# Kernel tuning notes

Hardware: AMD Instinct MI355X
Metric: run time of the kernel (lower is better)

## Reference

```python
import jax, jax.numpy as jnp
import numpy as np

N, D = 8192, 256
NUM_CLASSES = 100
WEIGHT = 1.0


def setup_inputs() -> dict:
    key = jax.random.key(0)
    k1, k2 = jax.random.split(key)
    predictions = jax.random.normal(k1, (N, D), dtype=jnp.float32)
    targets = jax.random.randint(k2, (N,), 0, NUM_CLASSES, dtype=jnp.int32)
    return {"predictions": predictions, "targets": targets}


def reference(predictions, targets):
    # Pairwise squared L2 via ||a||^2 + ||b||^2 - 2 a.b  -> [N, N]
    sq = jnp.sum(predictions * predictions, axis=1)
    d2 = sq[:, None] + sq[None, :] - 2.0 * (predictions @ predictions.T)
    dist = jnp.sqrt(jnp.maximum(d2, 0.0))  # torch.dist(p=2)

    n = predictions.shape[0]
    upper = jnp.triu(jnp.ones((n, n), dtype=bool), k=1)  # i < j pairs only
    same = targets[:, None] == targets[None, :]
    mask = upper & same

    num = jnp.sum(mask).astype(dist.dtype)
    loss = jnp.sum(jnp.where(mask, dist, 0.0)) / num
    return loss * WEIGHT
```

## Files before the change

### kernel.cpp

```cpp
#include <hip/hip_runtime.h>

#define N_CLS 100
#define D_DIM 256
#define MAX_M 112
#define ROW_SH 264
#define PANEL 48

typedef short bf16x8 __attribute__((ext_vector_type(8)));
typedef float f32x4  __attribute__((ext_vector_type(4)));

__device__ __forceinline__ unsigned short f2bf(float f) {
    unsigned int b = __float_as_uint(f);
    return (unsigned short)((b + 0x7FFFu + ((b >> 16) & 1u)) >> 16);
}

__global__ __launch_bounds__(1024) void k_prep(const int* __restrict__ targets, int n,
        int* __restrict__ offsets, int* __restrict__ bucket,
        double* __restrict__ npairs, double* __restrict__ gsum, int* __restrict__ gcount) {
    __shared__ int h[N_CLS], cur[N_CLS], offs[N_CLS + 1];
    const int t = threadIdx.x;
    if (t < N_CLS) h[t] = 0;
    __syncthreads();
    for (int i = t; i < n; i += 1024) atomicAdd(&h[targets[i]], 1);
    __syncthreads();
    if (t == 0) {
        int acc = 0; double p = 0.0;
        offs[0] = 0;
        for (int c = 0; c < N_CLS; ++c) {
            int m = h[c]; acc += m; offs[c + 1] = acc;
            p += (double)m * (double)(m - 1) * 0.5;
        }
        *npairs = p; *gsum = 0.0; *gcount = 0;
    }
    __syncthreads();
    if (t <= N_CLS) offsets[t] = offs[t];
    if (t < N_CLS) cur[t] = offs[t];
    __syncthreads();
    for (int i = t; i < n; i += 1024) {
        int c = targets[i];
        int pos = atomicAdd(&cur[c], 1);
        bucket[pos] = i;
    }
}

__device__ __forceinline__ void stage(const float* __restrict__ pred,
        const int* __restrict__ bucket, int base, int m, int cp0, int dslot, int cnt,
        short* tileS, float* sqs, int wave, int lane) {
    for (int r = wave; r < cnt; r += 8) {
        int cp = cp0 + r;
        float4 v = make_float4(0.f, 0.f, 0.f, 0.f);
        if (cp < m) {
            int g = bucket[base + cp];
            v = ((const float4*)(pred + (size_t)g * D_DIM))[lane];
        }
        short4 pk;
        pk.x = (short)f2bf(v.x); pk.y = (short)f2bf(v.y);
        pk.z = (short)f2bf(v.z); pk.w = (short)f2bf(v.w);
        *(short4*)&tileS[(dslot + r) * ROW_SH + lane * 4] = pk;
        float s = v.x * v.x + v.y * v.y + v.z * v.z + v.w * v.w;
        #pragma unroll
        for (int o = 32; o; o >>= 1) s += __shfl_xor(s, o, 64);
        if (lane == 0) sqs[dslot + r] = s;
    }
}

__device__ __forceinline__ float tile16(const short* tileS, const float* sqs,
        int a0, int b0, int ga0, int gb0, int m, int lane) {
    const int q = lane >> 4, l15 = lane & 15;
    const short* aP = &tileS[(a0 + l15) * ROW_SH + q * 8];
    const short* bP = &tileS[(b0 + l15) * ROW_SH + q * 8];
    f32x4 acc = {0.f, 0.f, 0.f, 0.f};
    #pragma unroll
    for (int ks = 0; ks < 8; ++ks) {
        bf16x8 af = *(const bf16x8*)(aP + ks * 32);
        bf16x8 bg = *(const bf16x8*)(bP + ks * 32);
        acc = __builtin_amdgcn_mfma_f32_16x16x32_bf16(af, bg, acc, 0, 0, 0);
    }
    float out = 0.f;
    #pragma unroll
    for (int rr = 0; rr < 4; ++rr) {
        int al = q * 4 + rr;
        int pi = ga0 + al, pj = gb0 + l15;
        float d2 = sqs[a0 + al] + sqs[b0 + l15] - 2.f * acc[rr];
        if (pj < m && pi < pj) out += sqrtf(fmaxf(d2, 0.f));
    }
    return out;
}

__global__ __launch_bounds__(512) void k_gram(const float* __restrict__ pred,
        const int* __restrict__ bucket, const int* __restrict__ offsets,
        const double* __restrict__ npairs, double* __restrict__ gsum,
        int* __restrict__ gcount, float* __restrict__ out) {
    __shared__ short tileS[MAX_M * ROW_SH];
    __shared__ float sqs[MAX_M];
    __shared__ float wsum[8];
    const int t = threadIdx.x, lane = t & 63, wave = t >> 6;
    const int c = blockIdx.x;
    const int base = offsets[c];
    const int m = offsets[c + 1] - base;
    float accum = 0.f;

    if (m <= MAX_M) {
        const int T = (m + 15) >> 4;
        stage(pred, bucket, base, m, 0, 0, T * 16, tileS, sqs, wave, lane);
        __syncthreads();
        const int np = T * (T + 1) / 2;
        for (int idx = wave; idx < np; idx += 8) {
            int ta = 0, r = idx;
            while (r >= T - ta) { r -= T - ta; ++ta; }
            int tb = ta + r;
            accum += tile16(tileS, sqs, ta * 16, tb * 16, ta * 16, tb * 16, m, lane);
        }
    } else {
        const int P = (m + PANEL - 1) / PANEL;
        for (int pi = 0; pi < P; ++pi)
        for (int pj = pi; pj < P; ++pj) {
            __syncthreads();
            stage(pred, bucket, base, m, pi * PANEL, 0,     PANEL, tileS, sqs, wave, lane);
            stage(pred, bucket, base, m, pj * PANEL, PANEL, PANEL, tileS, sqs, wave, lane);
            __syncthreads();
            for (int idx = wave; idx < 9; idx += 8) {
                int ta = idx / 3, tb = idx % 3;
                accum += tile16(tileS, sqs, ta * 16, PANEL + tb * 16,
                                pi * PANEL + ta * 16, pj * PANEL + tb * 16, m, lane);
            }
        }
    }

    #pragma unroll
    for (int o = 32; o; o >>= 1) accum += __shfl_xor(accum, o, 64);
    if (lane == 0) wsum[wave] = accum;
    __syncthreads();
    if (t == 0) {
        double bs = 0.0;
        #pragma unroll
        for (int w = 0; w < 8; ++w) bs += (double)wsum[w];
        atomicAdd(gsum, bs);
        __threadfence();
        int ticket = atomicAdd(gcount, 1);
        if (ticket == (int)gridDim.x - 1) {
            __threadfence();
            double s = atomicAdd(gsum, 0.0);
            out[0] = (float)(s / *npairs);
        }
    }
}

extern "C" void kernel_launch(void* const* d_in, const int* in_sizes, int n_in,
                              void* d_out, int out_size, void* d_ws, size_t ws_size,
                              hipStream_t stream) {
    const float* pred  = (const float*)d_in[0];
    const int* targets = (const int*)d_in[1];
    float* out         = (float*)d_out;
    const int n = in_sizes[1];

    char* ws = (char*)d_ws;
    size_t off = 0;
    double* npairs  = (double*)(ws + off); off += 8;
    double* gsum    = (double*)(ws + off); off += 8;
    int*    gcount  = (int*)(ws + off);    off += 8;
    int*    offsets = (int*)(ws + off);    off += (N_CLS + 1) * 4;
    int*    bucket  = (int*)(ws + off);

    k_prep<<<1, 1024, 0, stream>>>(targets, n, offsets, bucket, npairs, gsum, gcount);
    k_gram<<<N_CLS, 512, 0, stream>>>(pred, bucket, offsets, npairs, gsum, gcount, out);
}
```

Baseline: 80.09 us.

## Fold class bucketing into per-class gram blocks and add a final reduction kernel

```diff
diff --git a/kernel.cpp b/kernel.cpp
--- a/kernel.cpp
+++ b/kernel.cpp
@@ -14,43 +14,14 @@
     return (unsigned short)((b + 0x7FFFu + ((b >> 16) & 1u)) >> 16);
 }
 
-__global__ __launch_bounds__(1024) void k_prep(const int* __restrict__ targets, int n,
-        int* __restrict__ offsets, int* __restrict__ bucket,
-        double* __restrict__ npairs, double* __restrict__ gsum, int* __restrict__ gcount) {
-    __shared__ int h[N_CLS], cur[N_CLS], offs[N_CLS + 1];
-    const int t = threadIdx.x;
-    if (t < N_CLS) h[t] = 0;
-    __syncthreads();
-    for (int i = t; i < n; i += 1024) atomicAdd(&h[targets[i]], 1);
-    __syncthreads();
-    if (t == 0) {
-        int acc = 0; double p = 0.0;
-        offs[0] = 0;
-        for (int c = 0; c < N_CLS; ++c) {
-            int m = h[c]; acc += m; offs[c + 1] = acc;
-            p += (double)m * (double)(m - 1) * 0.5;
-        }
-        *npairs = p; *gsum = 0.0; *gcount = 0;
-    }
-    __syncthreads();
-    if (t <= N_CLS) offsets[t] = offs[t];
-    if (t < N_CLS) cur[t] = offs[t];
-    __syncthreads();
-    for (int i = t; i < n; i += 1024) {
-        int c = targets[i];
-        int pos = atomicAdd(&cur[c], 1);
-        bucket[pos] = i;
-    }
-}
-
 __device__ __forceinline__ void stage(const float* __restrict__ pred,
-        const int* __restrict__ bucket, int base, int m, int cp0, int dslot, int cnt,
+        const int* __restrict__ bkt, int m, int cp0, int dslot, int cnt,
         short* tileS, float* sqs, int wave, int lane) {
     for (int r = wave; r < cnt; r += 8) {
         int cp = cp0 + r;
         float4 v = make_float4(0.f, 0.f, 0.f, 0.f);
         if (cp < m) {
-            int g = bucket[base + cp];
+            int g = bkt[cp];
             v = ((const float4*)(pred + (size_t)g * D_DIM))[lane];
         }
         short4 pk;
@@ -88,21 +59,27 @@
 }
 
 __global__ __launch_bounds__(512) void k_gram(const float* __restrict__ pred,
-        const int* __restrict__ bucket, const int* __restrict__ offsets,
-        const double* __restrict__ npairs, double* __restrict__ gsum,
-        int* __restrict__ gcount, float* __restrict__ out) {
+        const int* __restrict__ targets, int n, int* __restrict__ bucket_g,
+        double* __restrict__ psum, double* __restrict__ pcnt) {
     __shared__ short tileS[MAX_M * ROW_SH];
     __shared__ float sqs[MAX_M];
     __shared__ float wsum[8];
+    __shared__ int cnt_s;
     const int t = threadIdx.x, lane = t & 63, wave = t >> 6;
     const int c = blockIdx.x;
-    const int base = offsets[c];
-    const int m = offsets[c + 1] - base;
+    int* bkt = bucket_g + (size_t)c * n;
+
+    if (t == 0) cnt_s = 0;
+    __syncthreads();
+    for (int i = t; i < n; i += 512)
+        if (targets[i] == c) bkt[atomicAdd(&cnt_s, 1)] = i;
+    __syncthreads();
+    const int m = cnt_s;
     float accum = 0.f;
 
     if (m <= MAX_M) {
         const int T = (m + 15) >> 4;
-        stage(pred, bucket, base, m, 0, 0, T * 16, tileS, sqs, wave, lane);
+        stage(pred, bkt, m, 0, 0, T * 16, tileS, sqs, wave, lane);
         __syncthreads();
         const int np = T * (T + 1) / 2;
         for (int idx = wave; idx < np; idx += 8) {
@@ -116,8 +93,8 @@
         for (int pi = 0; pi < P; ++pi)
         for (int pj = pi; pj < P; ++pj) {
             __syncthreads();
-            stage(pred, bucket, base, m, pi * PANEL, 0,     PANEL, tileS, sqs, wave, lane);
-            stage(pred, bucket, base, m, pj * PANEL, PANEL, PANEL, tileS, sqs, wave, lane);
+            stage(pred, bkt, m, pi * PANEL, 0,     PANEL, tileS, sqs, wave, lane);
+            stage(pred, bkt, m, pj * PANEL, PANEL, PANEL, tileS, sqs, wave, lane);
             __syncthreads();
             for (int idx = wave; idx < 9; idx += 8) {
                 int ta = idx / 3, tb = idx % 3;
@@ -135,15 +112,24 @@
         double bs = 0.0;
         #pragma unroll
         for (int w = 0; w < 8; ++w) bs += (double)wsum[w];
-        atomicAdd(gsum, bs);
-        __threadfence();
-        int ticket = atomicAdd(gcount, 1);
-        if (ticket == (int)gridDim.x - 1) {
-            __threadfence();
-            double s = atomicAdd(gsum, 0.0);
-            out[0] = (float)(s / *npairs);
-        }
+        psum[c] = bs;
+        pcnt[c] = (double)m * (double)(m - 1) * 0.5;
     }
+}
+
+__global__ void k_final(const double* __restrict__ psum, const double* __restrict__ pcnt,
+                        float* __restrict__ out) {
+    __shared__ double sh[128], ch[128];
+    int t = threadIdx.x;
+    double s = (t < N_CLS) ? psum[t] : 0.0;
+    double q = (t < N_CLS) ? pcnt[t] : 0.0;
+    sh[t] = s; ch[t] = q;
+    __syncthreads();
+    for (int w = 64; w; w >>= 1) {
+        if (t < w) { sh[t] += sh[t + w]; ch[t] += ch[t + w]; }
+        __syncthreads();
+    }
+    if (t == 0) out[0] = (float)(ch[0] > 0.0 ? sh[0] / ch[0] : 0.0);
 }
 
 extern "C" void kernel_launch(void* const* d_in, const int* in_sizes, int n_in,
@@ -156,12 +142,10 @@
 
     char* ws = (char*)d_ws;
     size_t off = 0;
-    double* npairs  = (double*)(ws + off); off += 8;
-    double* gsum    = (double*)(ws + off); off += 8;
-    int*    gcount  = (int*)(ws + off);    off += 8;
-    int*    offsets = (int*)(ws + off);    off += (N_CLS + 1) * 4;
-    int*    bucket  = (int*)(ws + off);
+    double* psum     = (double*)(ws + off); off += N_CLS * 8;
+    double* pcnt     = (double*)(ws + off); off += N_CLS * 8;
+    int*    bucket_g = (int*)(ws + off);
 
-    k_prep<<<1, 1024, 0, stream>>>(targets, n, offsets, bucket, npairs, gsum, gcount);
-    k_gram<<<N_CLS, 512, 0, stream>>>(pred, bucket, offsets, npairs, gsum, gcount, out);
+    k_gram<<<N_CLS, 512, 0, stream>>>(pred, targets, n, bucket_g, psum, pcnt);
+    k_final<<<1, 128, 0, stream>>>(psum, pcnt, out);
 }
```

Result: faster. 76.53 us (-4.4%).
